# Optimization experiments

Measured on AMD Instinct MI355X. Metric: run time of the kernel, lower is better.

## Reference

```python
import jax, jax.numpy as jnp
import numpy as np

N = 25000      # nodes
E = 400000     # edges
IN = 1024      # in_channels
FC = 128       # feature_channels
ADD = 20       # additional_channels
MID = (FC + ADD) // 4   # 37, fc1 output (heads=4)
OUT = 3
EPS = 1e-5
NEG_SLOPE = 0.01


def setup_inputs() -> dict:
    key = jax.random.key(0)
    ks = jax.random.split(key, 16)
    d = {}
    d["features"] = jax.random.normal(ks[0], (N, IN), dtype=jnp.float32)
    d["edges"] = jax.random.randint(ks[1], (2, E), 0, N, dtype=jnp.int64)
    d["edges2"] = jax.random.randint(ks[2], (2, 1000), 0, N, dtype=jnp.int64)
    d["edge_features"] = jax.random.normal(ks[3], (E, 1), dtype=jnp.float32)
    d["additional_feature"] = jax.random.normal(ks[4], (N, ADD), dtype=jnp.float32)
    # SAGEConv params: lin_l (neighbor path, with bias), lin_r (root path, no bias)
    s = 1.0 / np.sqrt(IN)
    d["Wl"] = jax.random.uniform(ks[5], (FC, IN), jnp.float32, -s, s)
    d["bl"] = jax.random.uniform(ks[6], (FC,), jnp.float32, -s, s)
    d["Wr"] = jax.random.uniform(ks[7], (FC, IN), jnp.float32, -s, s)
    s1 = 1.0 / np.sqrt(FC + ADD)
    d["W1"] = jax.random.uniform(ks[8], (MID, FC + ADD), jnp.float32, -s1, s1)
    d["b1"] = jax.random.uniform(ks[9], (MID,), jnp.float32, -s1, s1)
    s2 = 1.0 / np.sqrt(MID)
    d["W2"] = jax.random.uniform(ks[10], (OUT, MID), jnp.float32, -s2, s2)
    d["b2"] = jax.random.uniform(ks[11], (OUT,), jnp.float32, -s2, s2)
    # BatchNorm1d (eval mode -> running stats)
    d["gamma"] = jnp.ones((MID,), jnp.float32)
    d["beta"] = jnp.zeros((MID,), jnp.float32)
    d["run_mean"] = jax.random.normal(ks[12], (MID,), dtype=jnp.float32) * 0.1
    d["run_var"] = jnp.abs(jax.random.normal(ks[13], (MID,), dtype=jnp.float32)) * 0.1 + 1.0
    return d


def reference(features, edges, edges2, edge_features, additional_feature,
              Wl, bl, Wr, W1, b1, W2, b2, gamma, beta, run_mean, run_var):
    src, dst = edges[0], edges[1]  # PyG: messages flow source -> target
    # scatter-mean of neighbor features onto targets
    agg = jax.ops.segment_sum(features[src], dst, num_segments=N)        # [N, IN]
    deg = jax.ops.segment_sum(jnp.ones((E,), features.dtype), dst, num_segments=N)
    agg = agg / jnp.maximum(deg, 1.0)[:, None]
    # SAGEConv: lin_l(mean_neigh) + lin_r(x)
    x = agg @ Wl.T + bl + features @ Wr.T                                 # [N, FC]
    x = jnp.where(x >= 0, x, NEG_SLOPE * x)                               # leaky_relu
    # dropout is identity in eval mode
    x = jnp.concatenate([x, additional_feature], axis=1) @ W1.T + b1      # [N, MID]
    x = jnp.maximum(x, 0.0)                                               # relu
    x = gamma * (x - run_mean) * jax.lax.rsqrt(run_var + EPS) + beta      # BN eval
    return x @ W2.T + b2                                                  # [N, OUT]
```

## Files before the change

### kernel.cpp

```cpp
#include <hip/hip_runtime.h>

#define N_NODES 25000
#define N_EDGES 400000
#define IN_CH 1024
#define FC 128
#define ADD_CH 20
#define XCH 148
#define MID 37
#define OUT_CH 3
#define MAXDEG 64
#define CSTRIDE 16

typedef short bf16x8 __attribute__((ext_vector_type(8)));
typedef float f32x4 __attribute__((ext_vector_type(4)));
typedef unsigned int u32x4 __attribute__((ext_vector_type(4)));

__device__ __forceinline__ float bflo(unsigned int v) {
    return __builtin_bit_cast(float, v << 16);
}
__device__ __forceinline__ float bfhi(unsigned int v) {
    return __builtin_bit_cast(float, v & 0xffff0000u);
}
__device__ __forceinline__ unsigned int cvtpk(float a, float b) {
    unsigned int r;
    asm("v_cvt_pk_bf16_f32 %0, %1, %2" : "=v"(r) : "v"(a), "v"(b));
    return r;
}

__device__ __forceinline__ void gload16(const void* g, void* l) {
    __builtin_amdgcn_global_load_lds(
        (const __attribute__((address_space(1))) unsigned int*)g,
        (__attribute__((address_space(3))) unsigned int*)l,
        16, 0, 0);
}

#define WSWZ_B 16
#define ZERO_B 49

__global__ __launch_bounds__(512) void prep(const float* __restrict__ Wl,
                                            const float* __restrict__ Wr,
                                            ushort* __restrict__ Wpk,
                                            int* __restrict__ cursor) {
    int b = blockIdx.x, t = threadIdx.x;
    if (b < WSWZ_B) {
        int w = t >> 6, lane = t & 63, l15 = lane & 15, q8 = (lane >> 4) * 8;
        int ch = b * 16 + l15;
        const float* src = (ch < FC) ? (Wl + (size_t)ch * IN_CH)
                                     : (Wr + (size_t)(ch - FC) * IN_CH);
        #pragma unroll
        for (int j = 0; j < 4; ++j) {
            int kt = w * 4 + j;
            float4 lo = *(const float4*)(src + kt * 32 + q8);
            float4 hi = *(const float4*)(src + kt * 32 + q8 + 4);
            uint4 pk;
            pk.x = cvtpk(lo.x, lo.y); pk.y = cvtpk(lo.z, lo.w);
            pk.z = cvtpk(hi.x, hi.y); pk.w = cvtpk(hi.z, hi.w);
            ((uint4*)Wpk)[((size_t)kt * 16 + b) * 64 + lane] = pk;
        }
    } else {
        int i = (b - WSWZ_B) * 512 + t;
        if (i < N_NODES) {
            uint4 z = {0, 0, 0, 0};
            uint4* dst = (uint4*)(cursor + (size_t)i * CSTRIDE);
            dst[0] = z; dst[1] = z; dst[2] = z; dst[3] = z;
        }
    }
}

#define GEMM_B 391
#define BUILD_B 196

__global__ __launch_bounds__(512, 4) void gemm_build(const float* __restrict__ A,
                                                     const ushort* __restrict__ Wpk,
                                                     ushort* __restrict__ Py,
                                                     ushort* __restrict__ Pz,
                                                     const int* __restrict__ edges,
                                                     int* __restrict__ cursor,
                                                     int* __restrict__ col) {
    __shared__ uint4 LDS[3][512];
    int b = blockIdx.x, t = threadIdx.x;
    if (b >= GEMM_B) {
        int base = (b - GEMM_B) * 2048 + t;
        int src[4], dst[4], pos[4];
        #pragma unroll
        for (int k = 0; k < 4; ++k) {
            int e = base + k * 512;
            bool v = (e < N_EDGES);
            dst[k] = v ? edges[N_EDGES + e] : 0;
            src[k] = v ? edges[e] : 0;
        }
        #pragma unroll
        for (int k = 0; k < 4; ++k) {
            int e = base + k * 512;
            if (e < N_EDGES)
                pos[k] = atomicAdd(&cursor[(size_t)dst[k] * CSTRIDE], 1);
        }
        #pragma unroll
        for (int k = 0; k < 4; ++k) {
            int e = base + k * 512;
            if (e < N_EDGES && pos[k] < MAXDEG)
                col[dst[k] * MAXDEG + pos[k]] = src[k];
        }
        return;
    }
    int m0 = b * 64;
    int w = t >> 6, lane = t & 63;
    int l15 = lane & 15, q = lane >> 4;
    int tb = t & ~63;

    int ga = t >> 7, hq = (t >> 6) & 1;
    int nodeA = m0 + ga * 16 + l15;
    if (nodeA >= N_NODES) nodeA = N_NODES - 1;
    const float* Asrc = A + (size_t)nodeA * IN_CH + q * 8 + hq * 4;

    unsigned voff0 = (unsigned)(w * 128 + lane) * 16u;

    f32x4 acc[2][4] = {};
    u32x4 wA0, wA1, wB0, wB1, wC0, wC1;

    #define ISSUE_W(R0, R1, vo)                                                   \
        asm volatile("global_load_dwordx4 %0, %2, %3\n\t"                         \
                     "global_load_dwordx4 %1, %2, %3 offset:1024"                 \
                     : "=&v"(R0), "=&v"(R1) : "v"(vo), "s"(Wpk) : "memory");

    gload16(Asrc, &LDS[0][tb]);
    ISSUE_W(wA0, wA1, voff0)
    gload16(Asrc + 32, &LDS[1][tb]);
    { unsigned vo = voff0 + 16384u; ISSUE_W(wB0, wB1, vo) }

    #define COMPUTE(W0r, W1r, cb)                                                 \
    {                                                                             \
        bf16x8 wf0 = __builtin_bit_cast(bf16x8, W0r);                             \
        bf16x8 wf1 = __builtin_bit_cast(bf16x8, W1r);                             \
        _Pragma("unroll")                                                         \
        for (int g = 0; g < 4; ++g) {                                             \
            f32x4 lo = *(const f32x4*)&LDS[cb][g * 128 + lane];                   \
            f32x4 hi = *(const f32x4*)&LDS[cb][g * 128 + 64 + lane];              \
            uint4 pk_;                                                            \
            pk_.x = cvtpk(lo[0], lo[1]); pk_.y = cvtpk(lo[2], lo[3]);             \
            pk_.z = cvtpk(hi[0], hi[1]); pk_.w = cvtpk(hi[2], hi[3]);             \
            bf16x8 af = __builtin_bit_cast(bf16x8, pk_);                          \
            acc[0][g] = __builtin_amdgcn_mfma_f32_16x16x32_bf16(wf0, af, acc[0][g], 0, 0, 0); \
            acc[1][g] = __builtin_amdgcn_mfma_f32_16x16x32_bf16(wf1, af, acc[1][g], 0, 0, 0); \
        }                                                                         \
    }

    #define STEP(c, WS0, WS1, WC0, WC1, SBUF, CBUF)                               \
    {                                                                             \
        gload16(Asrc + (size_t)((c) + 2) * 32, &LDS[SBUF][tb]);                   \
        unsigned vo = voff0 + (unsigned)((c) + 2) * 16384u;                       \
        ISSUE_W(WS0, WS1, vo)                                                     \
        asm volatile("s_waitcnt vmcnt(6)" ::: "memory");                          \
        __builtin_amdgcn_sched_barrier(0);                                        \
        __builtin_amdgcn_s_barrier();                                             \
        __builtin_amdgcn_sched_barrier(0);                                        \
        COMPUTE(WC0, WC1, CBUF);                                                  \
        __builtin_amdgcn_s_barrier();                                             \
        __builtin_amdgcn_sched_barrier(0);                                        \
    }

    for (int cc = 0; cc < 30; cc += 3) {
        STEP(cc,     wC0, wC1, wA0, wA1, 2, 0)
        STEP(cc + 1, wA0, wA1, wB0, wB1, 0, 1)
        STEP(cc + 2, wB0, wB1, wC0, wC1, 1, 2)
    }
    asm volatile("s_waitcnt vmcnt(3)" ::: "memory");
    __builtin_amdgcn_sched_barrier(0);
    __builtin_amdgcn_s_barrier();
    __builtin_amdgcn_sched_barrier(0);
    COMPUTE(wA0, wA1, 0);
    asm volatile("s_waitcnt vmcnt(0)" ::: "memory");
    __builtin_amdgcn_sched_barrier(0);
    __builtin_amdgcn_s_barrier();
    __builtin_amdgcn_sched_barrier(0);
    COMPUTE(wB0, wB1, 1);
    #undef STEP
    #undef COMPUTE
    #undef ISSUE_W

    #pragma unroll
    for (int g = 0; g < 4; ++g) {
        int node = m0 + g * 16 + l15;
        if (node < N_NODES) {
            ushort* base = (w < 4) ? (Py + (size_t)node * FC + w * 32 + q * 4)
                                   : (Pz + (size_t)node * FC + (w - 4) * 32 + q * 4);
            #pragma unroll
            for (int cf = 0; cf < 2; ++cf) {
                f32x4 v = acc[cf][g];
                uint2 pk;
                pk.x = cvtpk(v[0], v[1]);
                pk.y = cvtpk(v[2], v[3]);
                *(uint2*)(base + cf * 16) = pk;
            }
        }
    }
}

__global__ __launch_bounds__(512) void fused_tail(const ushort* __restrict__ Py,
                                                  const ushort* __restrict__ Pz,
                                                  const int* __restrict__ deg,
                                                  const int* __restrict__ col,
                                                  const float* __restrict__ addf,
                                                  const float* __restrict__ bl,
                                                  const float* __restrict__ W1,
                                                  const float* __restrict__ b1,
                                                  const float* __restrict__ W2,
                                                  const float* __restrict__ b2,
                                                  const float* __restrict__ gamma,
                                                  const float* __restrict__ beta,
                                                  const float* __restrict__ rmean,
                                                  const float* __restrict__ rvar,
                                                  float* __restrict__ out) {
    __shared__ float W1s[XCH][MID + 3];
    __shared__ float xbuf[8][XCH + 4];
    __shared__ float hbuf[8][MID + 3];
    int t = threadIdx.x;
    for (int idx = t; idx < MID * XCH; idx += 512) {
        int j = idx / XCH, k = idx - j * XCH;
        W1s[k][j] = W1[idx];
    }
    __syncthreads();
    int w = t >> 6, lane = t & 63;
    int n = blockIdx.x * 8 + w;
    bool valid = (n < N_NODES);
    int d = valid ? deg[(size_t)n * CSTRIDE] : 0;
    if (d > MAXDEG) d = MAXDEG;
    int g = lane >> 4, c16 = lane & 15;
    float s[8] = {0.f, 0.f, 0.f, 0.f, 0.f, 0.f, 0.f, 0.f};
    if (d > 0) {
        int cidx = col[n * MAXDEG + (lane < d ? lane : 0)];
        for (int i = 0; i < d; i += 16) {
            int e[4];
            uint4 v[4];
            #pragma unroll
            for (int j = 0; j < 4; ++j) {
                int ee = i + g + j * 4;
                e[j] = __shfl(cidx, (ee < d) ? ee : 0);
            }
            #pragma unroll
            for (int j = 0; j < 4; ++j)
                v[j] = *(const uint4*)&Py[(size_t)e[j] * FC + c16 * 8];
            #pragma unroll
            for (int j = 0; j < 4; ++j) {
                if (i + g + j * 4 < d) {
                    s[0] += bflo(v[j].x); s[1] += bfhi(v[j].x);
                    s[2] += bflo(v[j].y); s[3] += bfhi(v[j].y);
                    s[4] += bflo(v[j].z); s[5] += bfhi(v[j].z);
                    s[6] += bflo(v[j].w); s[7] += bfhi(v[j].w);
                }
            }
        }
        #pragma unroll
        for (int r = 0; r < 8; ++r) {
            s[r] += __shfl_xor(s[r], 16);
            s[r] += __shfl_xor(s[r], 32);
        }
    }
    if (valid) {
        if (lane < 16) {
            #pragma unroll
            for (int r = 0; r < 8; ++r) xbuf[w][lane * 8 + r] = s[r];
        }
        float invd = 1.0f / (float)(d > 1 ? d : 1);
        unsigned int vr = *(const unsigned int*)&Pz[(size_t)n * FC + lane * 2];
        float x0 = xbuf[w][2 * lane] * invd + bl[2 * lane] + bflo(vr);
        float x1 = xbuf[w][2 * lane + 1] * invd + bl[2 * lane + 1] + bfhi(vr);
        x0 = (x0 >= 0.f) ? x0 : 0.01f * x0;
        x1 = (x1 >= 0.f) ? x1 : 0.01f * x1;
        xbuf[w][2 * lane] = x0;
        xbuf[w][2 * lane + 1] = x1;
        if (lane < ADD_CH) xbuf[w][FC + lane] = addf[(size_t)n * ADD_CH + lane];
        if (lane < MID) {
            float h = b1[lane];
            #pragma unroll 4
            for (int k = 0; k < XCH; ++k) h += W1s[k][lane] * xbuf[w][k];
            h = fmaxf(h, 0.0f);
            h = gamma[lane] * (h - rmean[lane]) * rsqrtf(rvar[lane] + 1e-5f) + beta[lane];
            hbuf[w][lane] = h;
        }
        if (lane < OUT_CH) {
            float o = b2[lane];
            #pragma unroll
            for (int j = 0; j < MID; ++j) o += W2[lane * MID + j] * hbuf[w][j];
            out[(size_t)n * OUT_CH + lane] = o;
        }
    }
}


extern "C" void kernel_launch(void* const* d_in, const int* in_sizes, int n_in,
                              void* d_out, int out_size, void* d_ws, size_t ws_size,
                              hipStream_t stream) {
    const float* features = (const float*)d_in[0];
    const int*   edges    = (const int*)d_in[1];
    const float* addf     = (const float*)d_in[4];
    const float* Wl       = (const float*)d_in[5];
    const float* bl       = (const float*)d_in[6];
    const float* Wr       = (const float*)d_in[7];
    const float* W1       = (const float*)d_in[8];
    const float* b1       = (const float*)d_in[9];
    const float* W2       = (const float*)d_in[10];
    const float* b2       = (const float*)d_in[11];
    const float* gamma    = (const float*)d_in[12];
    const float* beta     = (const float*)d_in[13];
    const float* rmean    = (const float*)d_in[14];
    const float* rvar     = (const float*)d_in[15];
    float* out = (float*)d_out;

    char* ws = (char*)d_ws;
    size_t off = 0;
    ushort* Py = (ushort*)(ws + off);     off += (size_t)N_NODES * FC * 2;
    ushort* Pz = (ushort*)(ws + off);     off += (size_t)N_NODES * FC * 2;
    ushort* Wpk = (ushort*)(ws + off);    off += (size_t)32 * 16 * 64 * 16;
    int* cursor = (int*)(ws + off);       off += (size_t)N_NODES * CSTRIDE * 4;
    int* col = (int*)(ws + off);          off += (size_t)N_NODES * MAXDEG * 4;

    prep<<<WSWZ_B + ZERO_B, 512, 0, stream>>>(Wl, Wr, Wpk, cursor);

    gemm_build<<<GEMM_B + BUILD_B, 512, 0, stream>>>(features, Wpk, Py, Pz,
                                                     edges, cursor, col);

    fused_tail<<<(N_NODES + 7) / 8, 512, 0, stream>>>(Py, Pz, cursor, col, addf, bl,
                                                      W1, b1, W2, b2, gamma, beta,
                                                      rmean, rvar, out);
}
```

Before: 270.4 us.

## Halve GEMM node tile to 32 rows with double-buffered 64-wide K steps

Changes the projection GEMM from 64-node tiles with triple-buffered 32-wide K chunks to 32-node tiles with double-buffered 64-wide K chunks. This doubles the number of GEMM blocks and raises the occupancy hint from 4 to 6. Each block now issues four weight loads per step and needs half the iterations, with fewer barriers per K element. The intent is more parallelism and latency hiding across the GPU. The cost is that each weight fragment is reused across only half as many nodes, which doubles total weight traffic, and the pipeline is shallower.

```diff
diff --git a/kernel.cpp b/kernel.cpp
--- a/kernel.cpp
+++ b/kernel.cpp
@@ -67,17 +67,17 @@
     }
 }
 
-#define GEMM_B 391
+#define GEMM_B 782
 #define BUILD_B 196
 
-__global__ __launch_bounds__(512, 4) void gemm_build(const float* __restrict__ A,
+__global__ __launch_bounds__(512, 6) void gemm_build(const float* __restrict__ A,
                                                      const ushort* __restrict__ Wpk,
                                                      ushort* __restrict__ Py,
                                                      ushort* __restrict__ Pz,
                                                      const int* __restrict__ edges,
                                                      int* __restrict__ cursor,
                                                      int* __restrict__ col) {
-    __shared__ uint4 LDS[3][512];
+    __shared__ uint4 LDS[2][512];
     int b = blockIdx.x, t = threadIdx.x;
     if (b >= GEMM_B) {
         int base = (b - GEMM_B) * 2048 + t;
@@ -103,94 +103,94 @@
         }
         return;
     }
-    int m0 = b * 64;
+    int m0 = b * 32;
     int w = t >> 6, lane = t & 63;
     int l15 = lane & 15, q = lane >> 4;
-    int tb = t & ~63;
-
-    int ga = t >> 7, hq = (t >> 6) & 1;
-    int nodeA = m0 + ga * 16 + l15;
+    int tb_ = t & ~63;
+
+    int sh = t >> 8, sg = (t >> 7) & 1, shq = (t >> 6) & 1;
+    int nodeA = m0 + sg * 16 + l15;
     if (nodeA >= N_NODES) nodeA = N_NODES - 1;
-    const float* Asrc = A + (size_t)nodeA * IN_CH + q * 8 + hq * 4;
-
-    unsigned voff0 = (unsigned)(w * 128 + lane) * 16u;
-
-    f32x4 acc[2][4] = {};
-    u32x4 wA0, wA1, wB0, wB1, wC0, wC1;
-
-    #define ISSUE_W(R0, R1, vo)                                                   \
-        asm volatile("global_load_dwordx4 %0, %2, %3\n\t"                         \
-                     "global_load_dwordx4 %1, %2, %3 offset:1024"                 \
-                     : "=&v"(R0), "=&v"(R1) : "v"(vo), "s"(Wpk) : "memory");
-
-    gload16(Asrc, &LDS[0][tb]);
-    ISSUE_W(wA0, wA1, voff0)
-    gload16(Asrc + 32, &LDS[1][tb]);
-    { unsigned vo = voff0 + 16384u; ISSUE_W(wB0, wB1, vo) }
-
-    #define COMPUTE(W0r, W1r, cb)                                                 \
+    const float* Asrc = A + (size_t)nodeA * IN_CH + sh * 32 + ((t >> 4) & 3) * 8 + shq * 4;
+
+    unsigned voff0 = (unsigned)(w * 2048 + lane * 16);
+
+    f32x4 acc[2][2] = {};
+    u32x4 wa0, wa1, wa2, wa3, wb0, wb1, wb2, wb3;
+
+    #define ISSUE_W(R0, R1, R2, R3, vo, vo2)                                      \
+        asm volatile("global_load_dwordx4 %0, %4, %5\n\t"                         \
+                     "global_load_dwordx4 %1, %4, %5 offset:1024\n\t"             \
+                     "global_load_dwordx4 %2, %6, %5\n\t"                         \
+                     "global_load_dwordx4 %3, %6, %5 offset:1024"                 \
+                     : "=&v"(R0), "=&v"(R1), "=&v"(R2), "=&v"(R3)                 \
+                     : "v"(vo), "s"(Wpk), "v"(vo2) : "memory");
+
+    gload16(Asrc, &LDS[0][tb_]);
+    { unsigned vo = voff0, vo2 = voff0 + 16384u; ISSUE_W(wa0, wa1, wa2, wa3, vo, vo2) }
+
+    #define COMPUTE(R0, R1, R2, R3, cb)                                           \
     {                                                                             \
-        bf16x8 wf0 = __builtin_bit_cast(bf16x8, W0r);                             \
-        bf16x8 wf1 = __builtin_bit_cast(bf16x8, W1r);                             \
         _Pragma("unroll")                                                         \
-        for (int g = 0; g < 4; ++g) {                                             \
-            f32x4 lo = *(const f32x4*)&LDS[cb][g * 128 + lane];                   \
-            f32x4 hi = *(const f32x4*)&LDS[cb][g * 128 + 64 + lane];              \
-            uint4 pk_;                                                            \
-            pk_.x = cvtpk(lo[0], lo[1]); pk_.y = cvtpk(lo[2], lo[3]);             \
-            pk_.z = cvtpk(hi[0], hi[1]); pk_.w = cvtpk(hi[2], hi[3]);             \
-            bf16x8 af = __builtin_bit_cast(bf16x8, pk_);                          \
-            acc[0][g] = __builtin_amdgcn_mfma_f32_16x16x32_bf16(wf0, af, acc[0][g], 0, 0, 0); \
-            acc[1][g] = __builtin_amdgcn_mfma_f32_16x16x32_bf16(wf1, af, acc[1][g], 0, 0, 0); \
+        for (int h = 0; h < 2; ++h) {                                             \
+            bf16x8 wf0 = __builtin_bit_cast(bf16x8, h ? R2 : R0);                 \
+            bf16x8 wf1 = __builtin_bit_cast(bf16x8, h ? R3 : R1);                 \
+            _Pragma("unroll")                                                     \
+            for (int g = 0; g < 2; ++g) {                                         \
+                f32x4 lo = *(const f32x4*)&LDS[cb][(h * 4 + g * 2 + 0) * 64 + lane]; \
+                f32x4 hi = *(const f32x4*)&LDS[cb][(h * 4 + g * 2 + 1) * 64 + lane]; \
+                uint4 pk_;                                                        \
+                pk_.x = cvtpk(lo[0], lo[1]); pk_.y = cvtpk(lo[2], lo[3]);         \
+                pk_.z = cvtpk(hi[0], hi[1]); pk_.w = cvtpk(hi[2], hi[3]);         \
+                bf16x8 af = __builtin_bit_cast(bf16x8, pk_);                      \
+                acc[0][g] = __builtin_amdgcn_mfma_f32_16x16x32_bf16(wf0, af, acc[0][g], 0, 0, 0); \
+                acc[1][g] = __builtin_amdgcn_mfma_f32_16x16x32_bf16(wf1, af, acc[1][g], 0, 0, 0); \
+            }                                                                     \
         }                                                                         \
     }
 
-    #define STEP(c, WS0, WS1, WC0, WC1, SBUF, CBUF)                               \
+    #define STEP(c, S0, S1, S2, S3, C0, C1, C2, C3, SBUF, CBUF)                   \
     {                                                                             \
-        gload16(Asrc + (size_t)((c) + 2) * 32, &LDS[SBUF][tb]);                   \
-        unsigned vo = voff0 + (unsigned)((c) + 2) * 16384u;                       \
-        ISSUE_W(WS0, WS1, vo)                                                     \
-        asm volatile("s_waitcnt vmcnt(6)" ::: "memory");                          \
+        gload16(Asrc + (size_t)((c) + 1) * 64, &LDS[SBUF][tb_]);                  \
+        unsigned vo = voff0 + (unsigned)((c) + 1) * 32768u;                       \
+        unsigned vo2 = vo + 16384u;                                               \
+        ISSUE_W(S0, S1, S2, S3, vo, vo2)                                          \
+        asm volatile("s_waitcnt vmcnt(5)" ::: "memory");                          \
         __builtin_amdgcn_sched_barrier(0);                                        \
         __builtin_amdgcn_s_barrier();                                             \
         __builtin_amdgcn_sched_barrier(0);                                        \
-        COMPUTE(WC0, WC1, CBUF);                                                  \
+        COMPUTE(C0, C1, C2, C3, CBUF);                                            \
         __builtin_amdgcn_s_barrier();                                             \
         __builtin_amdgcn_sched_barrier(0);                                        \
     }
 
-    for (int cc = 0; cc < 30; cc += 3) {
-        STEP(cc,     wC0, wC1, wA0, wA1, 2, 0)
-        STEP(cc + 1, wA0, wA1, wB0, wB1, 0, 1)
-        STEP(cc + 2, wB0, wB1, wC0, wC1, 1, 2)
-    }
-    asm volatile("s_waitcnt vmcnt(3)" ::: "memory");
-    __builtin_amdgcn_sched_barrier(0);
-    __builtin_amdgcn_s_barrier();
-    __builtin_amdgcn_sched_barrier(0);
-    COMPUTE(wA0, wA1, 0);
+    for (int cc = 0; cc < 14; cc += 2) {
+        STEP(cc,     wb0, wb1, wb2, wb3, wa0, wa1, wa2, wa3, 1, 0)
+        STEP(cc + 1, wa0, wa1, wa2, wa3, wb0, wb1, wb2, wb3, 0, 1)
+    }
+    STEP(14, wb0, wb1, wb2, wb3, wa0, wa1, wa2, wa3, 1, 0)
     asm volatile("s_waitcnt vmcnt(0)" ::: "memory");
     __builtin_amdgcn_sched_barrier(0);
     __builtin_amdgcn_s_barrier();
     __builtin_amdgcn_sched_barrier(0);
-    COMPUTE(wB0, wB1, 1);
+    COMPUTE(wb0, wb1, wb2, wb3, 1);
     #undef STEP
     #undef COMPUTE
     #undef ISSUE_W
 
     #pragma unroll
-    for (int g = 0; g < 4; ++g) {
+    for (int g = 0; g < 2; ++g) {
         int node = m0 + g * 16 + l15;
         if (node < N_NODES) {
-            ushort* base = (w < 4) ? (Py + (size_t)node * FC + w * 32 + q * 4)
-                                   : (Pz + (size_t)node * FC + (w - 4) * 32 + q * 4);
+            ushort* base = (w < 4) ? (Py + (size_t)node * FC + w * 32)
+                                   : (Pz + (size_t)node * FC + (w - 4) * 32);
             #pragma unroll
             for (int cf = 0; cf < 2; ++cf) {
                 f32x4 v = acc[cf][g];
                 uint2 pk;
                 pk.x = cvtpk(v[0], v[1]);
                 pk.y = cvtpk(v[2], v[3]);
-                *(uint2*)(base + cf * 16) = pk;
+                *(uint2*)(base + cf * 16 + q * 4) = pk;
             }
         }
     }
```

After: 273.8 us. About the same (+1.3%).
